# Performance work log

Hardware: AMD Instinct MI355X
Metric: run time of the kernel (lower is better)

The kernel has to match this reference:

```python
import jax, jax.numpy as jnp
import numpy as np

N = 32768        # out_features
K = 8192         # in_features
GROUP_SIZE = 128
G = K // GROUP_SIZE   # groups per row = 64
KP = K // 8           # packed bytes per row = 1024


def setup_inputs() -> dict:
    key = jax.random.key(0)
    k1, k2, k3 = jax.random.split(key, 3)
    x = jax.random.normal(k1, (1, K), dtype=jnp.float32).astype(jnp.float16)
    # packed sign bits: one uint8 holds 8 signs (bit i -> column k*8+i)
    packed_signs = jax.random.randint(k2, (N, KP), 0, 256, dtype=jnp.int32).astype(jnp.uint8)
    # per-(row, group) scales = mean |w| over each group of 128 weights (positive fp16)
    scales = (jax.random.uniform(k3, (N, G), dtype=jnp.float32) * 0.05 + 0.005).astype(jnp.float16)
    return {"x": x, "packed_signs": packed_signs, "scales": scales}


def _unpack_signs(packed_signs):
    # [N, KP] uint8 -> [N, K] float32 in {-1, +1}; bit i is weight column kb*8+i
    bits = (packed_signs[:, :, None] >> jnp.arange(8, dtype=jnp.uint8)[None, None, :]) & jnp.uint8(1)
    n, kp, _ = bits.shape
    return bits.reshape(n, kp * 8).astype(jnp.float32) * 2.0 - 1.0


def reference(x, packed_signs, scales):
    # out[b, n] = sum_k sign[n, k] * scale[n, k // group_size] * x[b, k]
    n, kp = packed_signs.shape
    k = kp * 8
    g = scales.shape[1]
    gs = k // g
    signs = _unpack_signs(packed_signs)                     # [N, K]
    xg = x.reshape(-1, g, gs).astype(jnp.float32)           # [B, G, gs]
    # per-group sign dot-products, then weight by the group scale
    partial = jnp.einsum('ngj,bgj->bng', signs.reshape(n, g, gs), xg)  # [B, N, G]
    out = jnp.einsum('bng,ng->bn', partial, scales.astype(jnp.float32))
    return out.astype(jnp.float16)                          # [1, N], fp16 like the kernel
```

## Files before the change

kernel.cpp:

```cpp
#include <hip/hip_runtime.h>
#include <hip/hip_fp16.h>

#define NROWS   32768
#define KTOT    8192
#define KP      1024
#define GROUPS  64

#define SLICE_W 1024
#define SLICE_I 128
#define NSLICES (KTOT / SLICE_W)
#define BLK     512
#define ROWS_PER_BLK 256
#define RCHUNKS (NROWS / ROWS_PER_BLK)
#define LUTW    136

__global__ __launch_bounds__(BLK, 8)
void bitlin_partials(const float* __restrict__ x,
                     const int* __restrict__ packed,
                     __half* __restrict__ pTh)
{
    __shared__ __align__(16) ushort lutU[SLICE_I * LUTW];

    const int s     = blockIdx.x & (NSLICES - 1);
    const int chunk = blockIdx.x >> 3;
    const int tid   = threadIdx.x;

    {
        const int pos = tid >> 2;
        const int oct = tid & 3;
        float xs[8];
#pragma unroll
        for (int i = 0; i < 8; ++i) xs[i] = x[s * SLICE_W + pos * 8 + i];
        float e = -xs[0] - xs[1] - xs[2] - xs[3] - xs[4]
                + ((oct & 1) ? xs[5] : -xs[5])
                + ((oct & 2) ? xs[6] : -xs[6])
                - xs[7];
        const float t0 = 2.f*xs[0], t1 = 2.f*xs[1], t2 = 2.f*xs[2],
                    t3 = 2.f*xs[3], t4 = 2.f*xs[4];
        ushort h[32];
#define HSET(i) h[i] = __half_as_ushort(__float2half_rn(e))
        HSET(0);
        e += t0; HSET(1);  e += t1; HSET(3);  e -= t0; HSET(2);
        e += t2; HSET(6);  e += t0; HSET(7);  e -= t1; HSET(5);  e -= t0; HSET(4);
        e += t3; HSET(12); e += t0; HSET(13); e += t1; HSET(15); e -= t0; HSET(14);
        e -= t2; HSET(10); e += t0; HSET(11); e -= t1; HSET(9);  e -= t0; HSET(8);
        e += t4; HSET(24); e += t0; HSET(25); e += t1; HSET(27); e -= t0; HSET(26);
        e += t2; HSET(30); e += t0; HSET(31); e -= t1; HSET(29); e -= t0; HSET(28);
        e -= t3; HSET(20); e += t0; HSET(21); e += t1; HSET(23); e -= t0; HSET(22);
        e -= t2; HSET(18); e += t0; HSET(19); e -= t1; HSET(17); e -= t0; HSET(16);
#undef HSET
#define PK(a,b) ((unsigned)h[a] | ((unsigned)h[b] << 16))
        uint4* dst = (uint4*)&lutU[pos * LUTW + oct * 32];
        dst[0] = make_uint4(PK( 0, 1), PK( 2, 3), PK( 4, 5), PK( 6, 7));
        dst[1] = make_uint4(PK( 8, 9), PK(10,11), PK(12,13), PK(14,15));
        dst[2] = make_uint4(PK(16,17), PK(18,19), PK(20,21), PK(22,23));
        dst[3] = make_uint4(PK(24,25), PK(26,27), PK(28,29), PK(30,31));
#undef PK
    }
    __syncthreads();

    const int lane = tid & 63;
    const int wave = tid >> 6;
    const int sub  = lane & 31;
    const int rsub = lane >> 5;
    const int rowBase = chunk * ROWS_PER_BLK + wave * 32;
    const int g = s * 8 + (sub >> 2);
    const ushort* lrow = &lutU[(sub * 4) * LUTW];

    const int4* __restrict__ p4 = (const int4*)packed;

#pragma unroll 4
    for (int t = 0; t < 16; ++t) {
        const int r = rowBase + t * 2 + rsub;
        const int4 v = p4[r * (KP / 4) + s * (SLICE_I / 4) + sub];
        const int bb[4] = { v.x & 255, v.y & 255, v.z & 255, v.w & 255 };
        float acc = 0.f;
#pragma unroll
        for (int c = 0; c < 4; ++c) {
            const int b   = bb[c];
            const int m   = b >> 7;
            const int idx = (b ^ (-m)) & 127;
            unsigned u = lrow[c * LUTW + idx];
            u ^= (unsigned)(m << 15);
            acc += __half2float(__ushort_as_half((ushort)u));
        }
        acc += __shfl_xor(acc, 1);
        acc += __shfl_xor(acc, 2);
        if ((sub & 3) == 0)
            pTh[g * NROWS + r] = __float2half_rn(acc);
    }
}

__global__ __launch_bounds__(512)
void bitlin_scale(const __half* __restrict__ pTh,
                  const float* __restrict__ scales,
                  float* __restrict__ out)
{
    __shared__ float s_s[64][65];
    __shared__ float s_part[64][9];

    const int tid     = threadIdx.x;
    const int lane    = tid & 63;
    const int wave    = tid >> 6;
    const int rowBase = blockIdx.x * 64;

    const float4* s4 = (const float4*)(scales + (size_t)rowBase * GROUPS);
#pragma unroll
    for (int i = 0; i < 2; ++i) {
        const int idx = i * 512 + tid;
        const float4 v = s4[idx];
        const int r = idx >> 4;
        const int c = (idx & 15) * 4;
        s_s[r][c + 0] = v.x;
        s_s[r][c + 1] = v.y;
        s_s[r][c + 2] = v.z;
        s_s[r][c + 3] = v.w;
    }
    __syncthreads();

    const int r = rowBase + lane;
    float acc = 0.f;
#pragma unroll
    for (int i = 0; i < 8; ++i) {
        const int g = wave * 8 + i;
        acc += __half2float(pTh[(size_t)g * NROWS + r]) * s_s[lane][g];
    }
    s_part[lane][wave] = acc;
    __syncthreads();

    if (wave == 0) {
        float a = 0.f;
#pragma unroll
        for (int w = 0; w < 8; ++w) a += s_part[lane][w];
        out[r] = a;
    }
}

__global__ __launch_bounds__(BLK, 4)
void bitlin_main_atomic(const float* __restrict__ x,
                        const int* __restrict__ packed,
                        const float* __restrict__ scales,
                        float* __restrict__ ws)
{
    __shared__ float lut[32][256];
    const int s     = blockIdx.x & 31;
    const int chunk = blockIdx.x >> 5;
    const int tid   = threadIdx.x;
    {
        const int pos = tid >> 4;
        const int b0  = (tid & 15) << 4;
        float xs[8];
#pragma unroll
        for (int i = 0; i < 8; ++i) xs[i] = x[s * 256 + pos * 8 + i];
#pragma unroll
        for (int b = 0; b < 16; ++b) {
            const int byte = b0 + b;
            float v = 0.f;
#pragma unroll
            for (int i = 0; i < 8; ++i)
                v += ((byte >> i) & 1) ? xs[i] : -xs[i];
            lut[pos][byte] = v;
        }
    }
    __syncthreads();

    const int lane = tid & 63;
    const int wave = tid >> 6;
    const int sub  = lane & 7;
    const int rsub = lane >> 3;
    const int rowBase = chunk * 512 + wave * 64;
    const int4* __restrict__ p4 = (const int4*)packed;

#pragma unroll
    for (int t = 0; t < 8; ++t) {
        const int r = rowBase + t * 8 + rsub;
        const int4 v = p4[r * (KP / 4) + s * 8 + sub];
        const float sc = scales[r * GROUPS + s * 2 + (sub >> 2)];
        const int pos0 = sub * 4;
        float acc = lut[pos0 + 0][v.x & 255]
                  + lut[pos0 + 1][v.y & 255]
                  + lut[pos0 + 2][v.z & 255]
                  + lut[pos0 + 3][v.w & 255];
        acc *= sc;
        acc += __shfl_xor(acc, 1);
        acc += __shfl_xor(acc, 2);
        acc += __shfl_xor(acc, 4);
        if (sub == 0) atomicAdd(&ws[r], acc);
    }
}

__global__ __launch_bounds__(512)
void bitlin_fin(const float* __restrict__ ws, float* __restrict__ out)
{
    const int i = blockIdx.x * blockDim.x + threadIdx.x;
    out[i] = ws[i];
}

extern "C" void kernel_launch(void* const* d_in, const int* in_sizes, int n_in,
                              void* d_out, int out_size, void* d_ws, size_t ws_size,
                              hipStream_t stream)
{
    const float* x      = (const float*)d_in[0];
    const int*   packed = (const int*)d_in[1];
    const float* scales = (const float*)d_in[2];

    const size_t pTh_bytes = (size_t)GROUPS * NROWS * sizeof(__half);

    if (ws_size >= pTh_bytes) {
        __half* pTh = (__half*)d_ws;
        bitlin_partials<<<dim3(NSLICES * RCHUNKS), dim3(BLK), 0, stream>>>(x, packed, pTh);
        bitlin_scale<<<dim3(NROWS / 64), dim3(512), 0, stream>>>(pTh, scales, (float*)d_out);
    } else {
        float* ws = (float*)d_ws;
        hipMemsetAsync(ws, 0, NROWS * sizeof(float), stream);
        bitlin_main_atomic<<<dim3(32 * (NROWS / 512)), dim3(BLK), 0, stream>>>(x, packed, scales, ws);
        bitlin_fin<<<dim3(NROWS / 512), dim3(512), 0, stream>>>(ws, (float*)d_out);
    }
}
```

Measured before the change: 30.26 us.

## Fuse partial-sum and scaling kernels into one block-per-64-rows kernel with prefetch

Replaces the two-kernel scheme, which wrote per-group fp16 partials to workspace and then scaled and reduced them, with one kernel. Each block owns 64 rows and walks all 8 K-slices, rebuilding the shared LUT per slice. It applies fp16-rounded scales in registers and prefetches the next slice's packed bits. This removes the 4 MB workspace round trip and a launch. In exchange every block rebuilds the LUT 8 times, there are two barriers per slice, and scales are now rounded to half.

```diff
diff --git a/kernel.cpp b/kernel.cpp
--- a/kernel.cpp
+++ b/kernel.cpp
@@ -8,212 +8,149 @@
 
 #define SLICE_W 1024
 #define SLICE_I 128
-#define NSLICES (KTOT / SLICE_W)
+#define NSLICES 8
 #define BLK     512
-#define ROWS_PER_BLK 256
-#define RCHUNKS (NROWS / ROWS_PER_BLK)
+#define ROWS_PER_BLK 64
+#define NBLOCKS (NROWS / ROWS_PER_BLK)
 #define LUTW    136
 
-__global__ __launch_bounds__(BLK, 8)
-void bitlin_partials(const float* __restrict__ x,
-                     const int* __restrict__ packed,
-                     __half* __restrict__ pTh)
+__global__ __launch_bounds__(BLK, 4)
+void bitlin_fused(const float* __restrict__ x,
+                  const int* __restrict__ packed,
+                  const float* __restrict__ scales,
+                  float* __restrict__ out)
 {
     __shared__ __align__(16) ushort lutU[SLICE_I * LUTW];
+    __shared__ ushort s_sh[ROWS_PER_BLK][66];
 
-    const int s     = blockIdx.x & (NSLICES - 1);
-    const int chunk = blockIdx.x >> 3;
-    const int tid   = threadIdx.x;
-
-    {
-        const int pos = tid >> 2;
-        const int oct = tid & 3;
-        float xs[8];
-#pragma unroll
-        for (int i = 0; i < 8; ++i) xs[i] = x[s * SLICE_W + pos * 8 + i];
-        float e = -xs[0] - xs[1] - xs[2] - xs[3] - xs[4]
-                + ((oct & 1) ? xs[5] : -xs[5])
-                + ((oct & 2) ? xs[6] : -xs[6])
-                - xs[7];
-        const float t0 = 2.f*xs[0], t1 = 2.f*xs[1], t2 = 2.f*xs[2],
-                    t3 = 2.f*xs[3], t4 = 2.f*xs[4];
-        ushort h[32];
-#define HSET(i) h[i] = __half_as_ushort(__float2half_rn(e))
-        HSET(0);
-        e += t0; HSET(1);  e += t1; HSET(3);  e -= t0; HSET(2);
-        e += t2; HSET(6);  e += t0; HSET(7);  e -= t1; HSET(5);  e -= t0; HSET(4);
-        e += t3; HSET(12); e += t0; HSET(13); e += t1; HSET(15); e -= t0; HSET(14);
-        e -= t2; HSET(10); e += t0; HSET(11); e -= t1; HSET(9);  e -= t0; HSET(8);
-        e += t4; HSET(24); e += t0; HSET(25); e += t1; HSET(27); e -= t0; HSET(26);
-        e += t2; HSET(30); e += t0; HSET(31); e -= t1; HSET(29); e -= t0; HSET(28);
-        e -= t3; HSET(20); e += t0; HSET(21); e += t1; HSET(23); e -= t0; HSET(22);
-        e -= t2; HSET(18); e += t0; HSET(19); e -= t1; HSET(17); e -= t0; HSET(16);
-#undef HSET
-#define PK(a,b) ((unsigned)h[a] | ((unsigned)h[b] << 16))
-        uint4* dst = (uint4*)&lutU[pos * LUTW + oct * 32];
-        dst[0] = make_uint4(PK( 0, 1), PK( 2, 3), PK( 4, 5), PK( 6, 7));
-        dst[1] = make_uint4(PK( 8, 9), PK(10,11), PK(12,13), PK(14,15));
-        dst[2] = make_uint4(PK(16,17), PK(18,19), PK(20,21), PK(22,23));
-        dst[3] = make_uint4(PK(24,25), PK(26,27), PK(28,29), PK(30,31));
-#undef PK
-    }
-    __syncthreads();
-
+    const int tid     = threadIdx.x;
+    const int rowBase = blockIdx.x * ROWS_PER_BLK;
     const int lane = tid & 63;
     const int wave = tid >> 6;
     const int sub  = lane & 31;
     const int rsub = lane >> 5;
-    const int rowBase = chunk * ROWS_PER_BLK + wave * 32;
-    const int g = s * 8 + (sub >> 2);
-    const ushort* lrow = &lutU[(sub * 4) * LUTW];
 
     const int4* __restrict__ p4 = (const int4*)packed;
 
-#pragma unroll 4
-    for (int t = 0; t < 16; ++t) {
-        const int r = rowBase + t * 2 + rsub;
-        const int4 v = p4[r * (KP / 4) + s * (SLICE_I / 4) + sub];
-        const int bb[4] = { v.x & 255, v.y & 255, v.z & 255, v.w & 255 };
-        float acc = 0.f;
+    int4 vbuf[4];
 #pragma unroll
-        for (int c = 0; c < 4; ++c) {
-            const int b   = bb[c];
-            const int m   = b >> 7;
-            const int idx = (b ^ (-m)) & 127;
-            unsigned u = lrow[c * LUTW + idx];
-            u ^= (unsigned)(m << 15);
-            acc += __half2float(__ushort_as_half((ushort)u));
-        }
-        acc += __shfl_xor(acc, 1);
-        acc += __shfl_xor(acc, 2);
-        if ((sub & 3) == 0)
-            pTh[g * NROWS + r] = __float2half_rn(acc);
+    for (int t = 0; t < 4; ++t) {
+        const int rl = wave * 8 + t * 2 + rsub;
+        vbuf[t] = p4[(size_t)(rowBase + rl) * (KP / 4) + sub];
     }
-}
 
-__global__ __launch_bounds__(512)
-void bitlin_scale(const __half* __restrict__ pTh,
-                  const float* __restrict__ scales,
-                  float* __restrict__ out)
-{
-    __shared__ float s_s[64][65];
-    __shared__ float s_part[64][9];
-
-    const int tid     = threadIdx.x;
-    const int lane    = tid & 63;
-    const int wave    = tid >> 6;
-    const int rowBase = blockIdx.x * 64;
-
-    const float4* s4 = (const float4*)(scales + (size_t)rowBase * GROUPS);
+    {
+        const float4* s4 = (const float4*)(scales + (size_t)rowBase * GROUPS);
 #pragma unroll
-    for (int i = 0; i < 2; ++i) {
-        const int idx = i * 512 + tid;
-        const float4 v = s4[idx];
-        const int r = idx >> 4;
-        const int c = (idx & 15) * 4;
-        s_s[r][c + 0] = v.x;
-        s_s[r][c + 1] = v.y;
-        s_s[r][c + 2] = v.z;
-        s_s[r][c + 3] = v.w;
-    }
-    __syncthreads();
-
-    const int r = rowBase + lane;
-    float acc = 0.f;
-#pragma unroll
-    for (int i = 0; i < 8; ++i) {
-        const int g = wave * 8 + i;
-        acc += __half2float(pTh[(size_t)g * NROWS + r]) * s_s[lane][g];
-    }
-    s_part[lane][wave] = acc;
-    __syncthreads();
-
-    if (wave == 0) {
-        float a = 0.f;
-#pragma unroll
-        for (int w = 0; w < 8; ++w) a += s_part[lane][w];
-        out[r] = a;
-    }
-}
-
-__global__ __launch_bounds__(BLK, 4)
-void bitlin_main_atomic(const float* __restrict__ x,
-                        const int* __restrict__ packed,
-                        const float* __restrict__ scales,
-                        float* __restrict__ ws)
-{
-    __shared__ float lut[32][256];
-    const int s     = blockIdx.x & 31;
-    const int chunk = blockIdx.x >> 5;
-    const int tid   = threadIdx.x;
-    {
-        const int pos = tid >> 4;
-        const int b0  = (tid & 15) << 4;
-        float xs[8];
-#pragma unroll
-        for (int i = 0; i < 8; ++i) xs[i] = x[s * 256 + pos * 8 + i];
-#pragma unroll
-        for (int b = 0; b < 16; ++b) {
-            const int byte = b0 + b;
-            float v = 0.f;
-#pragma unroll
-            for (int i = 0; i < 8; ++i)
-                v += ((byte >> i) & 1) ? xs[i] : -xs[i];
-            lut[pos][byte] = v;
+        for (int i = 0; i < 2; ++i) {
+            const int idx = i * 512 + tid;
+            const float4 v = s4[idx];
+            const int r = idx >> 4;
+            const int c = (idx & 15) * 4;
+            s_sh[r][c + 0] = __half_as_ushort(__float2half_rn(v.x));
+            s_sh[r][c + 1] = __half_as_ushort(__float2half_rn(v.y));
+            s_sh[r][c + 2] = __half_as_ushort(__float2half_rn(v.z));
+            s_sh[r][c + 3] = __half_as_ushort(__float2half_rn(v.w));
         }
     }
-    __syncthreads();
 
-    const int lane = tid & 63;
-    const int wave = tid >> 6;
-    const int sub  = lane & 7;
-    const int rsub = lane >> 3;
-    const int rowBase = chunk * 512 + wave * 64;
-    const int4* __restrict__ p4 = (const int4*)packed;
+    float acc[4] = {0.f, 0.f, 0.f, 0.f};
 
+    for (int s = 0; s < NSLICES; ++s) {
+        {
+            const int pos = tid >> 2;
+            const int oct = tid & 3;
+            float xs[8];
 #pragma unroll
-    for (int t = 0; t < 8; ++t) {
-        const int r = rowBase + t * 8 + rsub;
-        const int4 v = p4[r * (KP / 4) + s * 8 + sub];
-        const float sc = scales[r * GROUPS + s * 2 + (sub >> 2)];
-        const int pos0 = sub * 4;
-        float acc = lut[pos0 + 0][v.x & 255]
-                  + lut[pos0 + 1][v.y & 255]
-                  + lut[pos0 + 2][v.z & 255]
-                  + lut[pos0 + 3][v.w & 255];
-        acc *= sc;
-        acc += __shfl_xor(acc, 1);
-        acc += __shfl_xor(acc, 2);
-        acc += __shfl_xor(acc, 4);
-        if (sub == 0) atomicAdd(&ws[r], acc);
+            for (int i = 0; i < 8; ++i) xs[i] = x[s * SLICE_W + pos * 8 + i];
+            float e = -xs[0] - xs[1] - xs[2] - xs[3] - xs[4]
+                    + ((oct & 1) ? xs[5] : -xs[5])
+                    + ((oct & 2) ? xs[6] : -xs[6])
+                    - xs[7];
+            const float t0 = 2.f*xs[0], t1 = 2.f*xs[1], t2 = 2.f*xs[2],
+                        t3 = 2.f*xs[3], t4 = 2.f*xs[4];
+            ushort h[32];
+#define HSET(i) h[i] = __half_as_ushort(__float2half_rn(e))
+            HSET(0);
+            e += t0; HSET(1);  e += t1; HSET(3);  e -= t0; HSET(2);
+            e += t2; HSET(6);  e += t0; HSET(7);  e -= t1; HSET(5);  e -= t0; HSET(4);
+            e += t3; HSET(12); e += t0; HSET(13); e += t1; HSET(15); e -= t0; HSET(14);
+            e -= t2; HSET(10); e += t0; HSET(11); e -= t1; HSET(9);  e -= t0; HSET(8);
+            e += t4; HSET(24); e += t0; HSET(25); e += t1; HSET(27); e -= t0; HSET(26);
+            e += t2; HSET(30); e += t0; HSET(31); e -= t1; HSET(29); e -= t0; HSET(28);
+            e -= t3; HSET(20); e += t0; HSET(21); e += t1; HSET(23); e -= t0; HSET(22);
+            e -= t2; HSET(18); e += t0; HSET(19); e -= t1; HSET(17); e -= t0; HSET(16);
+#undef HSET
+#define PK(a,b) ((unsigned)h[a] | ((unsigned)h[b] << 16))
+            uint4* dst = (uint4*)&lutU[pos * LUTW + oct * 32];
+            dst[0] = make_uint4(PK( 0, 1), PK( 2, 3), PK( 4, 5), PK( 6, 7));
+            dst[1] = make_uint4(PK( 8, 9), PK(10,11), PK(12,13), PK(14,15));
+            dst[2] = make_uint4(PK(16,17), PK(18,19), PK(20,21), PK(22,23));
+            dst[3] = make_uint4(PK(24,25), PK(26,27), PK(28,29), PK(30,31));
+#undef PK
+        }
+        __syncthreads();
+
+        int4 vnext[4];
+        if (s < NSLICES - 1) {
+#pragma unroll
+            for (int t = 0; t < 4; ++t) {
+                const int rl = wave * 8 + t * 2 + rsub;
+                vnext[t] = p4[(size_t)(rowBase + rl) * (KP / 4)
+                              + (s + 1) * (SLICE_I / 4) + sub];
+            }
+        }
+
+        const ushort* lrow = &lutU[(sub * 4) * LUTW];
+#pragma unroll
+        for (int t = 0; t < 4; ++t) {
+            const int rl = wave * 8 + t * 2 + rsub;
+            const int bb[4] = { vbuf[t].x & 255, vbuf[t].y & 255,
+                                vbuf[t].z & 255, vbuf[t].w & 255 };
+            float part = 0.f;
+#pragma unroll
+            for (int c = 0; c < 4; ++c) {
+                const int b   = bb[c];
+                const int m   = b >> 7;
+                const int idx = (b ^ (-m)) & 127;
+                unsigned u = lrow[c * LUTW + idx];
+                u ^= (unsigned)(m << 15);
+                part += __half2float(__ushort_as_half((ushort)u));
+            }
+            part += __shfl_xor(part, 1);
+            part += __shfl_xor(part, 2);
+            const float sc =
+                __half2float(__ushort_as_half(s_sh[rl][s * 8 + (sub >> 2)]));
+            float v = part * sc;
+            v += __shfl_xor(v, 4);
+            v += __shfl_xor(v, 8);
+            v += __shfl_xor(v, 16);
+            acc[t] += v;
+        }
+        __syncthreads();
+
+        if (s < NSLICES - 1) {
+#pragma unroll
+            for (int t = 0; t < 4; ++t) vbuf[t] = vnext[t];
+        }
     }
-}
 
-__global__ __launch_bounds__(512)
-void bitlin_fin(const float* __restrict__ ws, float* __restrict__ out)
-{
-    const int i = blockIdx.x * blockDim.x + threadIdx.x;
-    out[i] = ws[i];
+    if (sub == 0) {
+#pragma unroll
+        for (int t = 0; t < 4; ++t)
+            out[rowBase + wave * 8 + t * 2 + rsub] = acc[t];
+    }
 }
 
 extern "C" void kernel_launch(void* const* d_in, const int* in_sizes, int n_in,
                               void* d_out, int out_size, void* d_ws, size_t ws_size,
                               hipStream_t stream)
 {
+    (void)d_ws; (void)ws_size; (void)n_in; (void)in_sizes; (void)out_size;
     const float* x      = (const float*)d_in[0];
     const int*   packed = (const int*)d_in[1];
     const float* scales = (const float*)d_in[2];
 
-    const size_t pTh_bytes = (size_t)GROUPS * NROWS * sizeof(__half);
-
-    if (ws_size >= pTh_bytes) {
-        __half* pTh = (__half*)d_ws;
-        bitlin_partials<<<dim3(NSLICES * RCHUNKS), dim3(BLK), 0, stream>>>(x, packed, pTh);
-        bitlin_scale<<<dim3(NROWS / 64), dim3(512), 0, stream>>>(pTh, scales, (float*)d_out);
-    } else {
-        float* ws = (float*)d_ws;
-        hipMemsetAsync(ws, 0, NROWS * sizeof(float), stream);
-        bitlin_main_atomic<<<dim3(32 * (NROWS / 512)), dim3(BLK), 0, stream>>>(x, packed, scales, ws);
-        bitlin_fin<<<dim3(NROWS / 512), dim3(512), 0, stream>>>(ws, (float*)d_out);
-    }
+    bitlin_fused<<<dim3(NBLOCKS), dim3(BLK), 0, stream>>>(
+        x, packed, scales, (float*)d_out);
 }
```

Result: slower. 31.37 us (+3.7%).
